# Performance work log

Measured on AMD Instinct MI355X. Metric: run time of the kernel, lower is better.

The kernel has to match this reference:

```python
import jax, jax.numpy as jnp
import numpy as np

MAX_VALUE = 127.0  # signed 8-bit: 2**(8-1)-1


def _quantize_int8(t, amax):
    # per-tensor symmetric quantization: round(x * 127/amax), clamped to [-127, 127]
    scale = MAX_VALUE / amax
    return jnp.clip(jnp.round(t * scale), -MAX_VALUE, MAX_VALUE).astype(jnp.int8)


def setup_inputs() -> dict:
    key = jax.random.key(0)
    k1, k2, k3 = jax.random.split(key, 3)
    N, K, M = 8192, 4096, 4096
    x = jax.random.normal(k1, (N, K), dtype=jnp.float32)
    weight = jax.random.normal(k2, (M, K), dtype=jnp.float32) * (1.0 / np.sqrt(K))
    bias = jax.random.normal(k3, (M,), dtype=jnp.float32) * (1.0 / np.sqrt(K))
    return {"x": x, "weight": weight, "bias": bias}


def reference(x, weight, bias):
    # amax from max-abs calibration (per-tensor), as TensorQuantizer would hold
    amax = jnp.max(jnp.abs(x))
    amax_w = jnp.max(jnp.abs(weight))
    qi = _quantize_int8(x, amax)          # [N, K] int8
    qw = _quantize_int8(weight, amax_w)   # [M, K] int8
    acc = jnp.matmul(qi.astype(jnp.int32), qw.astype(jnp.int32).T)  # [N, M] int32
    # dequant: output / ((max/amax) * (max/amax_w)), then bias
    dequant = (amax * amax_w) / (MAX_VALUE * MAX_VALUE)
    return acc.astype(jnp.float32) * dequant + bias
```

## Files before the change

kernel.cpp:

```cpp
#include <hip/hip_runtime.h>

#define K_DIM 4096
#define N_DIM 8192
#define M_DIM 4096

typedef int v4i __attribute__((ext_vector_type(4)));

__global__ void amax2_kernel(const float4* __restrict__ x,
                             const float4* __restrict__ w,
                             unsigned* __restrict__ scal) {
  const int XB = 2048, WB = 1024;
  const float4* p;
  int n4, b, nb;
  unsigned* out;
  if (blockIdx.x < XB) {
    p = x; n4 = N_DIM * K_DIM / 4; out = scal + 0; b = blockIdx.x; nb = XB;
  } else {
    p = w; n4 = M_DIM * K_DIM / 4; out = scal + 1; b = blockIdx.x - XB; nb = WB;
  }
  int tid = b * blockDim.x + threadIdx.x;
  int stride = nb * blockDim.x;
  float m = 0.f;
  for (int i = tid; i < n4; i += stride) {
    float4 v = p[i];
    m = fmaxf(m, fmaxf(fmaxf(fabsf(v.x), fabsf(v.y)),
                       fmaxf(fabsf(v.z), fabsf(v.w))));
  }
#pragma unroll
  for (int off = 32; off > 0; off >>= 1)
    m = fmaxf(m, __shfl_down(m, off));
  __shared__ float sm[4];
  int lane = threadIdx.x & 63, wv = threadIdx.x >> 6;
  if (lane == 0) sm[wv] = m;
  __syncthreads();
  if (threadIdx.x == 0) {
    m = fmaxf(fmaxf(sm[0], sm[1]), fmaxf(sm[2], sm[3]));
    atomicMax(out, __float_as_uint(m));
  }
}

__device__ __forceinline__ unsigned pack4(float4 v, float s) {
  int q0 = (int)fminf(fmaxf(rintf(v.x * s), -127.f), 127.f);
  int q1 = (int)fminf(fmaxf(rintf(v.y * s), -127.f), 127.f);
  int q2 = (int)fminf(fmaxf(rintf(v.z * s), -127.f), 127.f);
  int q3 = (int)fminf(fmaxf(rintf(v.w * s), -127.f), 127.f);
  return (unsigned)(q0 & 255) | ((unsigned)(q1 & 255) << 8) |
         ((unsigned)(q2 & 255) << 16) | ((unsigned)(q3 & 255) << 24);
}

__global__ void quant2_kernel(const float4* __restrict__ x,
                              const float4* __restrict__ w,
                              int4* __restrict__ qx, int4* __restrict__ qw,
                              const unsigned* __restrict__ scal) {
  const int XB = 2048, WB = 1024;
  const float4* in;
  int4* out;
  int n16, b, nb;
  float amax;
  if (blockIdx.x < XB) {
    in = x; out = qx; n16 = N_DIM * K_DIM / 16; b = blockIdx.x; nb = XB;
    amax = __uint_as_float(scal[0]);
  } else {
    in = w; out = qw; n16 = M_DIM * K_DIM / 16; b = blockIdx.x - XB; nb = WB;
    amax = __uint_as_float(scal[1]);
  }
  float s = 127.0f / amax;
  int tid = b * blockDim.x + threadIdx.x;
  int stride = nb * blockDim.x;
  for (int i = tid; i < n16; i += stride) {
    float4 v0 = in[4 * i + 0];
    float4 v1 = in[4 * i + 1];
    float4 v2 = in[4 * i + 2];
    float4 v3 = in[4 * i + 3];
    int4 o;
    o.x = (int)pack4(v0, s);
    o.y = (int)pack4(v1, s);
    o.z = (int)pack4(v2, s);
    o.w = (int)pack4(v3, s);
    out[i] = o;
  }
}

__device__ __forceinline__ void gld_lds16(const void* g, void* l) {
  __builtin_amdgcn_global_load_lds(
      (const __attribute__((address_space(1))) void*)g,
      (__attribute__((address_space(3))) void*)l, 16, 0, 0);
}

__global__ __launch_bounds__(256, 2) void gemm_i8(
    const signed char* __restrict__ A,
    const signed char* __restrict__ B,
    const float* __restrict__ bias,
    float* __restrict__ out,
    const unsigned* __restrict__ scal)
{
  __shared__ signed char la[128 * 128];
  __shared__ signed char lb[128 * 128];

  const int tid = threadIdx.x;
  const int lane = tid & 63;
  const int w = tid >> 6;
  const int wr = (w & 1) * 64;
  const int wc = (w >> 1) * 64;
  const long r0 = (long)blockIdx.x * 128;
  const long c0 = (long)blockIdx.y * 128;

  const int srow = tid >> 3;
  const int gcol = ((tid & 7) ^ (srow & 7)) * 16;
  const signed char* ga = A + (r0 + srow) * K_DIM + gcol;
  const signed char* gb = B + (c0 + srow) * K_DIM + gcol;

  v4i acc[4][4];
#pragma unroll
  for (int i = 0; i < 4; ++i)
#pragma unroll
    for (int j = 0; j < 4; ++j) acc[i][j] = (v4i){0, 0, 0, 0};

  const int fr = lane & 15;
  const int fq = lane >> 4;
  const int sa = fr & 7;

  for (int k0 = 0; k0 < K_DIM; k0 += 128) {
#pragma unroll
    for (int p = 0; p < 4; ++p) {
      gld_lds16(ga + (long)p * 32 * K_DIM + k0, la + p * 4096 + tid * 16);
      gld_lds16(gb + (long)p * 32 * K_DIM + k0, lb + p * 4096 + tid * 16);
    }
    __syncthreads();

#pragma unroll
    for (int ks = 0; ks < 2; ++ks) {
      v4i av[4], bv[4];
#pragma unroll
      for (int i = 0; i < 4; ++i)
        av[i] = *(const v4i*)(la + (wr + i * 16 + fr) * 128 +
                              (((ks * 4 + fq) ^ sa) * 16));
#pragma unroll
      for (int j = 0; j < 4; ++j)
        bv[j] = *(const v4i*)(lb + (wc + j * 16 + fr) * 128 +
                              (((ks * 4 + fq) ^ sa) * 16));
#pragma unroll
      for (int i = 0; i < 4; ++i)
#pragma unroll
        for (int j = 0; j < 4; ++j)
          acc[i][j] = __builtin_amdgcn_mfma_i32_16x16x64_i8(av[i], bv[j],
                                                            acc[i][j], 0, 0, 0);
    }
    __syncthreads();
  }

  const float dq =
      (__uint_as_float(scal[0]) * __uint_as_float(scal[1])) / 16129.0f;
  float bs[4];
#pragma unroll
  for (int j = 0; j < 4; ++j) bs[j] = bias[c0 + wc + j * 16 + fr];

#pragma unroll
  for (int i = 0; i < 4; ++i) {
    const long rbase = r0 + wr + i * 16 + fq * 4;
#pragma unroll
    for (int j = 0; j < 4; ++j) {
      const long c = c0 + wc + j * 16 + fr;
#pragma unroll
      for (int t = 0; t < 4; ++t) {
        out[(rbase + t) * (long)M_DIM + c] = (float)acc[i][j][t] * dq + bs[j];
      }
    }
  }
}

extern "C" void kernel_launch(void* const* d_in, const int* in_sizes, int n_in,
                              void* d_out, int out_size, void* d_ws, size_t ws_size,
                              hipStream_t stream) {
  const float* x = (const float*)d_in[0];
  const float* wt = (const float*)d_in[1];
  const float* bias = (const float*)d_in[2];
  float* out = (float*)d_out;

  unsigned* scal = (unsigned*)d_ws;
  signed char* qx = (signed char*)d_ws + 256;
  signed char* qw = qx + (long)N_DIM * K_DIM;

  hipMemsetAsync(d_ws, 0, 16, stream);

  amax2_kernel<<<3072, 256, 0, stream>>>((const float4*)x, (const float4*)wt,
                                         scal);
  quant2_kernel<<<3072, 256, 0, stream>>>((const float4*)x, (const float4*)wt,
                                          (int4*)qx, (int4*)qw, scal);

  dim3 grid(N_DIM / 128, M_DIM / 128);
  gemm_i8<<<grid, 256, 0, stream>>>(qx, qw, bias, out, scal);
}
```

Measured before the change: 441.1 us.

## Switch GEMM to 32x32x32 int8 MFMA and unroll amax/quant loops

```diff
diff --git a/kernel.cpp b/kernel.cpp
--- a/kernel.cpp
+++ b/kernel.cpp
@@ -5,6 +5,7 @@
 #define M_DIM 4096
 
 typedef int v4i __attribute__((ext_vector_type(4)));
+typedef int v16i __attribute__((ext_vector_type(16)));
 
 __global__ void amax2_kernel(const float4* __restrict__ x,
                              const float4* __restrict__ w,
@@ -18,10 +19,25 @@
   } else {
     p = w; n4 = M_DIM * K_DIM / 4; out = scal + 1; b = blockIdx.x - XB; nb = WB;
   }
-  int tid = b * blockDim.x + threadIdx.x;
-  int stride = nb * blockDim.x;
+  const int stride = nb * blockDim.x;
+  int i = b * blockDim.x + threadIdx.x;
   float m = 0.f;
-  for (int i = tid; i < n4; i += stride) {
+  for (; i + 3 * stride < n4; i += 4 * stride) {
+    float4 v0 = p[i];
+    float4 v1 = p[i + stride];
+    float4 v2 = p[i + 2 * stride];
+    float4 v3 = p[i + 3 * stride];
+    float m0 = fmaxf(fmaxf(fabsf(v0.x), fabsf(v0.y)),
+                     fmaxf(fabsf(v0.z), fabsf(v0.w)));
+    float m1 = fmaxf(fmaxf(fabsf(v1.x), fabsf(v1.y)),
+                     fmaxf(fabsf(v1.z), fabsf(v1.w)));
+    float m2 = fmaxf(fmaxf(fabsf(v2.x), fabsf(v2.y)),
+                     fmaxf(fabsf(v2.z), fabsf(v2.w)));
+    float m3 = fmaxf(fmaxf(fabsf(v3.x), fabsf(v3.y)),
+                     fmaxf(fabsf(v3.z), fabsf(v3.w)));
+    m = fmaxf(m, fmaxf(fmaxf(m0, m1), fmaxf(m2, m3)));
+  }
+  for (; i < n4; i += stride) {
     float4 v = p[i];
     m = fmaxf(m, fmaxf(fmaxf(fabsf(v.x), fabsf(v.y)),
                        fmaxf(fabsf(v.z), fabsf(v.w))));
@@ -50,35 +66,35 @@
 
 __global__ void quant2_kernel(const float4* __restrict__ x,
                               const float4* __restrict__ w,
-                              int4* __restrict__ qx, int4* __restrict__ qw,
+                              unsigned* __restrict__ qx,
+                              unsigned* __restrict__ qw,
                               const unsigned* __restrict__ scal) {
   const int XB = 2048, WB = 1024;
   const float4* in;
-  int4* out;
-  int n16, b, nb;
+  unsigned* out;
+  int n4, b, nb;
   float amax;
   if (blockIdx.x < XB) {
-    in = x; out = qx; n16 = N_DIM * K_DIM / 16; b = blockIdx.x; nb = XB;
+    in = x; out = qx; n4 = N_DIM * K_DIM / 4; b = blockIdx.x; nb = XB;
     amax = __uint_as_float(scal[0]);
   } else {
-    in = w; out = qw; n16 = M_DIM * K_DIM / 16; b = blockIdx.x - XB; nb = WB;
+    in = w; out = qw; n4 = M_DIM * K_DIM / 4; b = blockIdx.x - XB; nb = WB;
     amax = __uint_as_float(scal[1]);
   }
-  float s = 127.0f / amax;
-  int tid = b * blockDim.x + threadIdx.x;
-  int stride = nb * blockDim.x;
-  for (int i = tid; i < n16; i += stride) {
-    float4 v0 = in[4 * i + 0];
-    float4 v1 = in[4 * i + 1];
-    float4 v2 = in[4 * i + 2];
-    float4 v3 = in[4 * i + 3];
-    int4 o;
-    o.x = (int)pack4(v0, s);
-    o.y = (int)pack4(v1, s);
-    o.z = (int)pack4(v2, s);
-    o.w = (int)pack4(v3, s);
-    out[i] = o;
-  }
+  const float s = 127.0f / amax;
+  const int stride = nb * blockDim.x;
+  int i = b * blockDim.x + threadIdx.x;
+  for (; i + 3 * stride < n4; i += 4 * stride) {
+    float4 v0 = in[i];
+    float4 v1 = in[i + stride];
+    float4 v2 = in[i + 2 * stride];
+    float4 v3 = in[i + 3 * stride];
+    out[i] = pack4(v0, s);
+    out[i + stride] = pack4(v1, s);
+    out[i + 2 * stride] = pack4(v2, s);
+    out[i + 3 * stride] = pack4(v3, s);
+  }
+  for (; i < n4; i += stride) out[i] = pack4(in[i], s);
 }
 
 __device__ __forceinline__ void gld_lds16(const void* g, void* l) {
@@ -110,15 +126,17 @@
   const signed char* ga = A + (r0 + srow) * K_DIM + gcol;
   const signed char* gb = B + (c0 + srow) * K_DIM + gcol;
 
-  v4i acc[4][4];
-#pragma unroll
-  for (int i = 0; i < 4; ++i)
-#pragma unroll
-    for (int j = 0; j < 4; ++j) acc[i][j] = (v4i){0, 0, 0, 0};
-
-  const int fr = lane & 15;
-  const int fq = lane >> 4;
-  const int sa = fr & 7;
+  v16i acc[2][2];
+#pragma unroll
+  for (int i = 0; i < 2; ++i)
+#pragma unroll
+    for (int j = 0; j < 2; ++j)
+#pragma unroll
+      for (int t = 0; t < 16; ++t) acc[i][j][t] = 0;
+
+  const int ln = lane & 31;
+  const int hk = lane >> 5;
+  const int sa = ln & 7;
 
   for (int k0 = 0; k0 < K_DIM; k0 += 128) {
 #pragma unroll
@@ -129,21 +147,20 @@
     __syncthreads();
 
 #pragma unroll
-    for (int ks = 0; ks < 2; ++ks) {
-      v4i av[4], bv[4];
-#pragma unroll
-      for (int i = 0; i < 4; ++i)
-        av[i] = *(const v4i*)(la + (wr + i * 16 + fr) * 128 +
-                              (((ks * 4 + fq) ^ sa) * 16));
-#pragma unroll
-      for (int j = 0; j < 4; ++j)
-        bv[j] = *(const v4i*)(lb + (wc + j * 16 + fr) * 128 +
-                              (((ks * 4 + fq) ^ sa) * 16));
-#pragma unroll
-      for (int i = 0; i < 4; ++i)
-#pragma unroll
-        for (int j = 0; j < 4; ++j)
-          acc[i][j] = __builtin_amdgcn_mfma_i32_16x16x64_i8(av[i], bv[j],
+    for (int ks = 0; ks < 4; ++ks) {
+      const int ck = ks * 2 + hk;
+      v4i av[2], bv[2];
+#pragma unroll
+      for (int i = 0; i < 2; ++i)
+        av[i] = *(const v4i*)(la + (wr + i * 32 + ln) * 128 + ((ck ^ sa) * 16));
+#pragma unroll
+      for (int j = 0; j < 2; ++j)
+        bv[j] = *(const v4i*)(lb + (wc + j * 32 + ln) * 128 + ((ck ^ sa) * 16));
+#pragma unroll
+      for (int i = 0; i < 2; ++i)
+#pragma unroll
+        for (int j = 0; j < 2; ++j)
+          acc[i][j] = __builtin_amdgcn_mfma_i32_32x32x32_i8(av[i], bv[j],
                                                             acc[i][j], 0, 0, 0);
     }
     __syncthreads();
@@ -151,19 +168,19 @@
 
   const float dq =
       (__uint_as_float(scal[0]) * __uint_as_float(scal[1])) / 16129.0f;
-  float bs[4];
-#pragma unroll
-  for (int j = 0; j < 4; ++j) bs[j] = bias[c0 + wc + j * 16 + fr];
-
-#pragma unroll
-  for (int i = 0; i < 4; ++i) {
-    const long rbase = r0 + wr + i * 16 + fq * 4;
-#pragma unroll
-    for (int j = 0; j < 4; ++j) {
-      const long c = c0 + wc + j * 16 + fr;
-#pragma unroll
-      for (int t = 0; t < 4; ++t) {
-        out[(rbase + t) * (long)M_DIM + c] = (float)acc[i][j][t] * dq + bs[j];
+  float bs[2];
+#pragma unroll
+  for (int j = 0; j < 2; ++j) bs[j] = bias[c0 + wc + j * 32 + ln];
+
+#pragma unroll
+  for (int i = 0; i < 2; ++i) {
+#pragma unroll
+    for (int j = 0; j < 2; ++j) {
+      const long c = c0 + wc + j * 32 + ln;
+#pragma unroll
+      for (int reg = 0; reg < 16; ++reg) {
+        const long r = r0 + wr + i * 32 + (reg & 3) + 8 * (reg >> 2) + 4 * hk;
+        out[r * (long)M_DIM + c] = (float)acc[i][j][reg] * dq + bs[j];
       }
     }
   }
@@ -186,7 +203,7 @@
   amax2_kernel<<<3072, 256, 0, stream>>>((const float4*)x, (const float4*)wt,
                                          scal);
   quant2_kernel<<<3072, 256, 0, stream>>>((const float4*)x, (const float4*)wt,
-                                          (int4*)qx, (int4*)qw, scal);
+                                          (unsigned*)qx, (unsigned*)qw, scal);
 
   dim3 grid(N_DIM / 128, M_DIM / 128);
   gemm_i8<<<grid, 256, 0, stream>>>(qx, qw, bias, out, scal);
```

Measured after the change: 448.8 us. About the same (+1.7%).
